# Performance work log

Measured on AMD Instinct MI355X. Metric: run time of the kernel, lower is better.

The kernel has to match this reference:

```python
import jax, jax.numpy as jnp
import numpy as np
import math

B, S, H, NH, NKV, HD = 1, 2048, 4096, 32, 8, 128
ROPE_THETA = 10000.0


def setup_inputs() -> dict:
    key = jax.random.key(0)
    ks = jax.random.split(key, 16)
    hidden_states = jax.random.normal(ks[0], (B, S, H), jnp.float32) * 0.02
    Wq = jax.random.normal(ks[1], (NH * HD, H), jnp.float32) * 0.02
    Wk = jax.random.normal(ks[2], (NKV * HD, H), jnp.float32) * 0.02
    Wv = jax.random.normal(ks[3], (NKV * HD, H), jnp.float32) * 0.02
    Wo = jax.random.normal(ks[4], (H, NH * HD), jnp.float32) * 0.02
    # RoPE cos/sin, HF Llama convention: emb = concat(freqs, freqs)
    inv_freq = 1.0 / (ROPE_THETA ** (jnp.arange(0, HD, 2, dtype=jnp.float32) / HD))
    pos = jnp.arange(S, dtype=jnp.float32)
    freqs = pos[:, None] * inv_freq[None, :]              # [S, HD/2]
    emb = jnp.concatenate([freqs, freqs], axis=-1)        # [S, HD]
    cos = jnp.cos(emb)[None]                              # [1, S, HD]
    sin = jnp.sin(emb)[None]
    # additive causal mask [B, 1, S, S]
    causal = jnp.tril(jnp.ones((S, S), dtype=bool))
    attention_mask = jnp.where(causal, 0.0, -1e9).astype(jnp.float32)[None, None]
    # reorder permutations (as written by GPTQ act-order reordering)
    perm = lambda k, n: jax.random.permutation(k, n).astype(jnp.int32)
    return {
        'hidden_states': hidden_states, 'Wq': Wq, 'Wk': Wk, 'Wv': Wv, 'Wo': Wo,
        'cos': cos, 'sin': sin, 'attention_mask': attention_mask,
        'q_order_col': perm(ks[5], H), 'q_order_row': perm(ks[6], NH * HD),
        'k_order_col': perm(ks[7], H), 'k_order_row': perm(ks[8], NKV * HD),
        'v_order_col': perm(ks[9], H), 'v_order_row': perm(ks[10], NKV * HD),
        'o_order_col': perm(ks[11], NH * HD), 'o_order_row': perm(ks[12], H),
    }


def _rotate_half(x):
    x1, x2 = jnp.split(x, 2, axis=-1)
    return jnp.concatenate([-x2, x1], axis=-1)


def reference(hidden_states, Wq, Wk, Wv, Wo, cos, sin, attention_mask,
              q_order_col, q_order_row, k_order_col, k_order_row,
              v_order_col, v_order_row, o_order_col, o_order_row):
    bsz, q_len, _ = hidden_states.shape
    # permuted projections: gather cols of input, GEMM, gather rows of output
    q = hidden_states[:, :, q_order_col] @ Wq.T
    q = q[:, :, q_order_row]
    k = hidden_states[:, :, k_order_col] @ Wk.T
    k = k[:, :, k_order_row]
    v = hidden_states[:, :, v_order_col] @ Wv.T
    v = v[:, :, v_order_row]
    q = q.reshape(bsz, q_len, NH, HD).transpose(0, 2, 1, 3)   # [B,NH,S,HD]
    k = k.reshape(bsz, q_len, NKV, HD).transpose(0, 2, 1, 3)  # [B,NKV,S,HD]
    v = v.reshape(bsz, q_len, NKV, HD).transpose(0, 2, 1, 3)
    # RoPE
    c = cos[:, None, :, :]  # [1,1,S,HD]
    s = sin[:, None, :, :]
    q = q * c + _rotate_half(q) * s
    k = k * c + _rotate_half(k) * s
    # repeat_kv for GQA
    rep = NH // NKV
    k = jnp.repeat(k, rep, axis=1)  # [B,NH,S,HD]
    v = jnp.repeat(v, rep, axis=1)
    # eager attention: full score matrix, fp32 softmax
    scores = jnp.einsum('bhqd,bhkd->bhqk', q, k) / math.sqrt(HD)
    scores = scores + attention_mask
    probs = jax.nn.softmax(scores.astype(jnp.float32), axis=-1).astype(q.dtype)
    # dropout p=0.0 (eval) -> identity
    attn = jnp.einsum('bhqk,bhkd->bhqd', probs, v)
    attn = attn.transpose(0, 2, 1, 3).reshape(bsz, q_len, NH * HD)
    out = attn[:, :, o_order_col] @ Wo.T
    out = out[:, :, o_order_row]
    return out
```

## Files before the change

### kernel.cpp

```cpp
#include <hip/hip_runtime.h>

typedef unsigned short u16;
typedef unsigned char u8;
typedef __bf16 bf16x8 __attribute__((ext_vector_type(8)));
typedef float f32x4 __attribute__((ext_vector_type(4)));
typedef int i32x4 __attribute__((ext_vector_type(4)));
typedef int i32x8 __attribute__((ext_vector_type(8)));

__device__ __forceinline__ u16 f2bf(float f) {
    unsigned u = __float_as_uint(f);
    unsigned r = (u + 0x7fffu + ((u >> 16) & 1u)) >> 16;
    return (u16)r;
}
__device__ __forceinline__ float bf2f(u16 h) {
    return __uint_as_float(((unsigned)h) << 16);
}
__device__ __forceinline__ unsigned pack_bf2(float lo, float hi) {
    unsigned a = __float_as_uint(hi) + 0x8000u;
    unsigned b = __float_as_uint(lo) + 0x8000u;
    return __builtin_amdgcn_perm(a, b, 0x07060302u);
}
__device__ __forceinline__ unsigned pack_fp8x4(float a, float b, float c, float d) {
    unsigned w = __builtin_amdgcn_cvt_pk_fp8_f32(a, b, 0, false);
    w = __builtin_amdgcn_cvt_pk_fp8_f32(c, d, w, true);
    return w;
}
__device__ __forceinline__ void async_copy16(const void* g, void* l) {
    __builtin_amdgcn_global_load_lds((__attribute__((address_space(1))) void*)(void*)g,
                                     (__attribute__((address_space(3))) void*)l, 16, 0, 0);
}

#define FP8_SCALE 64.0f
#define FP8_UNSCALE (1.0f / 4096.0f)


__global__ void inv4_k(const int* __restrict__ q, const int* __restrict__ k,
                       const int* __restrict__ v, const int* __restrict__ o,
                       int* __restrict__ invq, int* __restrict__ invk,
                       int* __restrict__ invv, int* __restrict__ invo) {
    int i = blockIdx.x * 256 + threadIdx.x;
    int a = i >> 12, j = i & 4095;
    const int* p = a == 0 ? q : a == 1 ? k : a == 2 ? v : o;
    int* inv = a == 0 ? invq : a == 1 ? invk : a == 2 ? invv : invo;
    inv[p[j]] = j;
}

__global__ __launch_bounds__(256) void permw4_k(
    const float* __restrict__ Wq, const float* __restrict__ Wk,
    const float* __restrict__ Wv, const float* __restrict__ Wo,
    const int* __restrict__ qor, const int* __restrict__ kor,
    const int* __restrict__ vor, const int* __restrict__ oor,
    const int* __restrict__ invq, const int* __restrict__ invk,
    const int* __restrict__ invv, const int* __restrict__ invo,
    u8* __restrict__ Wqkf8, u16* __restrict__ Wvp, u16* __restrict__ Wop) {
    __shared__ float rowbuf[4096];
    int j = blockIdx.x;
    const float* W; const int* rp; const int* inv; int row; int f8;
    u8* out8 = nullptr; u16* out16 = nullptr;
    if (j < 4096)      { W = Wq; rp = qor; inv = invq; row = j;        out8 = Wqkf8 + (size_t)j * 4096; f8 = 1; }
    else if (j < 5120) { W = Wk; rp = kor; inv = invk; row = j - 4096; out8 = Wqkf8 + (size_t)j * 4096; f8 = 1; }
    else if (j < 6144) { W = Wv; rp = vor; inv = invv; row = j - 5120; out16 = Wvp + (size_t)(j - 5120) * 4096; f8 = 0; }
    else               { W = Wo; rp = oor; inv = invo; row = j - 6144; out16 = Wop + (size_t)(j - 6144) * 4096; f8 = 0; }
    const float4* wr4 = (const float4*)(W + (size_t)rp[row] * 4096);
#pragma unroll
    for (int t = 0; t < 4; t++)
        ((float4*)rowbuf)[threadIdx.x + t * 256] = wr4[threadIdx.x + t * 256];
    __syncthreads();
    if (f8) {
        int t = threadIdx.x;
        const int4* inv4p = (const int4*)inv;
        float v[16];
#pragma unroll
        for (int u = 0; u < 4; u++) {
            int4 ix = inv4p[t * 4 + u];
            v[4 * u + 0] = rowbuf[ix.x] * FP8_SCALE;
            v[4 * u + 1] = rowbuf[ix.y] * FP8_SCALE;
            v[4 * u + 2] = rowbuf[ix.z] * FP8_SCALE;
            v[4 * u + 3] = rowbuf[ix.w] * FP8_SCALE;
        }
        uint4 wv;
        wv.x = pack_fp8x4(v[0], v[1], v[2], v[3]);
        wv.y = pack_fp8x4(v[4], v[5], v[6], v[7]);
        wv.z = pack_fp8x4(v[8], v[9], v[10], v[11]);
        wv.w = pack_fp8x4(v[12], v[13], v[14], v[15]);
        int tb = (t & ~7) | ((t & 7) ^ (j & 7));
        ((uint4*)out8)[tb] = wv;
    } else {
        unsigned* o32 = (unsigned*)out16;
        const int2* inv2 = (const int2*)inv;
#pragma unroll
        for (int t = 0; t < 8; t++) {
            int c = threadIdx.x + t * 256;
            int2 ij = inv2[c];
            o32[c] = pack_bf2(rowbuf[ij.x], rowbuf[ij.y]);
        }
    }
}

__global__ __launch_bounds__(256) void cvt_k(const float* __restrict__ x,
                                             u16* __restrict__ Xb,
                                             u8* __restrict__ Xf8) {
    int row = blockIdx.x;
    int t = threadIdx.x;
    const float4* src = (const float4*)(x + (size_t)row * 4096);
    float v[16];
#pragma unroll
    for (int u = 0; u < 4; u++) {
        float4 a = src[t * 4 + u];
        v[4 * u + 0] = a.x; v[4 * u + 1] = a.y; v[4 * u + 2] = a.z; v[4 * u + 3] = a.w;
    }
    uint4 b0, b1;
    b0.x = pack_bf2(v[0], v[1]);  b0.y = pack_bf2(v[2], v[3]);
    b0.z = pack_bf2(v[4], v[5]);  b0.w = pack_bf2(v[6], v[7]);
    b1.x = pack_bf2(v[8], v[9]);  b1.y = pack_bf2(v[10], v[11]);
    b1.z = pack_bf2(v[12], v[13]); b1.w = pack_bf2(v[14], v[15]);
    uint4* ob = (uint4*)(Xb + (size_t)row * 4096);
    ob[t * 2] = b0;
    ob[t * 2 + 1] = b1;
    uint4 w8;
    w8.x = pack_fp8x4(v[0] * FP8_SCALE, v[1] * FP8_SCALE, v[2] * FP8_SCALE, v[3] * FP8_SCALE);
    w8.y = pack_fp8x4(v[4] * FP8_SCALE, v[5] * FP8_SCALE, v[6] * FP8_SCALE, v[7] * FP8_SCALE);
    w8.z = pack_fp8x4(v[8] * FP8_SCALE, v[9] * FP8_SCALE, v[10] * FP8_SCALE, v[11] * FP8_SCALE);
    w8.w = pack_fp8x4(v[12] * FP8_SCALE, v[13] * FP8_SCALE, v[14] * FP8_SCALE, v[15] * FP8_SCALE);
    int tb = (t & ~7) | ((t & 7) ^ (row & 7));
    ((uint4*)(Xf8 + (size_t)row * 4096))[tb] = w8;
}

__global__ __launch_bounds__(256) void rope_tr_k(u16* __restrict__ X,
                                                 const float* __restrict__ cosv,
                                                 const float* __restrict__ sinv,
                                                 const float* __restrict__ Vpart,
                                                 u16* __restrict__ Vt) {
    __shared__ u16 t[64][65];
    if (blockIdx.x < 20480) {
        int tt = blockIdx.x * 256 + threadIdx.x;
        int d = tt & 63;
        int rest = tt >> 6;
        int head = rest % 40;
        int s = rest / 40;
        size_t base = (size_t)s * 6144 + head * 128 + d;
        float x1 = bf2f(X[base]), x2 = bf2f(X[base + 64]);
        float c1 = cosv[s * 128 + d], s1 = sinv[s * 128 + d];
        float c2 = cosv[s * 128 + d + 64], s2 = sinv[s * 128 + d + 64];
        float sc = head < 32 ? 0.08838834764831845f : 1.0f;
        X[base]      = f2bf((x1 * c1 - x2 * s1) * sc);
        X[base + 64] = f2bf((x2 * c2 + x1 * s2) * sc);
    } else {
        int bx = blockIdx.x - 20480;
        int s0 = (bx & 31) * 64, c0 = (bx >> 5) * 64;
        int x = threadIdx.x & 63, y4 = threadIdx.x >> 6;
        const float* Vp0 = Vpart;
        const float* Vp1 = Vpart + (size_t)2048 * 1024;
        for (int i = 0; i < 16; i++) {
            int r = y4 * 16 + i;
            size_t idx = (size_t)(s0 + r) * 1024 + c0 + x;
            t[r][x] = f2bf(Vp0[idx] + Vp1[idx]);
        }
        __syncthreads();
        for (int i = 0; i < 16; i++) {
            int r = y4 * 16 + i;
            int xk = 4 * (x & 15) + (x >> 4);
            Vt[(size_t)(c0 + r) * 2048 + s0 + xk] = t[x][r];
        }
    }
}


__global__ __launch_bounds__(256) void gemm_qkv_k(const u8* __restrict__ Xf8,
                                                  const u16* __restrict__ Xb,
                                                  const u8* __restrict__ Wqk,
                                                  const u16* __restrict__ Wv,
                                                  u16* __restrict__ QKV,
                                                  float* __restrict__ Vpart) {
    __shared__ u8 lds[32768];
    const int tid = threadIdx.x;
    const int w = tid >> 6, lane = tid & 63;
    const int quad = lane >> 4, l16 = lane & 15;
    const int bm0 = blockIdx.y * 128;
    const int wm = (w >> 1) * 64, wn = (w & 1) * 64;
    if (blockIdx.x < 40) {
        const int bn0 = blockIdx.x * 128;
        u8* ldsA = lds;
        u8* ldsB = lds + 16384;
        const u8* Ag = Xf8 + (size_t)(bm0 + w * 32 + (lane >> 3)) * 4096 + (lane & 7) * 16;
        const u8* Bg = Wqk + (size_t)(bn0 + w * 32 + (lane >> 3)) * 4096 + (lane & 7) * 16;
        u8* la = ldsA + w * 32 * 128;
        u8* lb = ldsB + w * 32 * 128;
        const int swz = l16 & 7;
        f32x4 acc[4][4] = {};
        for (int k0 = 0; k0 < 4096; k0 += 128) {
#pragma unroll
            for (int t = 0; t < 4; t++) async_copy16(Ag + (size_t)t * 8 * 4096 + k0, la + t * 1024);
#pragma unroll
            for (int t = 0; t < 4; t++) async_copy16(Bg + (size_t)t * 8 * 4096 + k0, lb + t * 1024);
            __syncthreads();
            i32x8 af[4], bf[4];
#pragma unroll
            for (int i = 0; i < 4; i++) {
                int r = wm + i * 16 + l16;
                union { i32x8 v8; i32x4 v4[2]; } u;
                u.v4[0] = *(const i32x4*)&ldsA[r * 128 + ((quad * 2) ^ swz) * 16];
                u.v4[1] = *(const i32x4*)&ldsA[r * 128 + ((quad * 2 + 1) ^ swz) * 16];
                af[i] = u.v8;
            }
#pragma unroll
            for (int j = 0; j < 4; j++) {
                int r = wn + j * 16 + l16;
                union { i32x8 v8; i32x4 v4[2]; } u;
                u.v4[0] = *(const i32x4*)&ldsB[r * 128 + ((quad * 2) ^ swz) * 16];
                u.v4[1] = *(const i32x4*)&ldsB[r * 128 + ((quad * 2 + 1) ^ swz) * 16];
                bf[j] = u.v8;
            }
#pragma unroll
            for (int i = 0; i < 4; i++)
#pragma unroll
                for (int j = 0; j < 4; j++)
                    acc[i][j] = __builtin_amdgcn_mfma_scale_f32_16x16x128_f8f6f4(
                        af[i], bf[j], acc[i][j], 0, 0,
                        0, 0x7F7F7F7F, 0, 0x7F7F7F7F);
            __syncthreads();
        }
#pragma unroll
        for (int i = 0; i < 4; i++) {
            const int row = bm0 + wm + i * 16 + quad * 4;
#pragma unroll
            for (int j = 0; j < 4; j++) {
                const int col = bn0 + wn + j * 16 + l16;
#pragma unroll
                for (int r = 0; r < 4; r++)
                    QKV[(size_t)(row + r) * 6144 + col] = f2bf(acc[i][j][r] * FP8_UNSCALE);
            }
        }
    } else {
        const int vx = blockIdx.x - 40;
        const int bn0 = (vx & 7) * 128;
        const int kslice = vx >> 3;
        const int kb = kslice * 2048;
        u16* lds_a0 = (u16*)lds;
        u16* lds_a1 = (u16*)(lds + 8192);
        u16* lds_b0 = (u16*)(lds + 16384);
        u16* lds_b1 = (u16*)(lds + 24576);
        const int r0 = w * 16 + (lane >> 2);
        const int c0 = (lane & 3) * 8;
        const u16* Ag = Xb + (size_t)(bm0 + r0) * 4096 + kb + c0;
        const u16* Bg = Wv + (size_t)(bn0 + r0) * 4096 + kb + c0;
        f32x4 acc[4][4] = {};
        for (int k0 = 0; k0 < 2048; k0 += 64) {
            async_copy16(Ag + k0,                         lds_a0 + w * 512);
            async_copy16(Ag + (size_t)64 * 4096 + k0,     lds_a0 + (w + 4) * 512);
            async_copy16(Ag + k0 + 32,                    lds_a1 + w * 512);
            async_copy16(Ag + (size_t)64 * 4096 + k0 + 32, lds_a1 + (w + 4) * 512);
            async_copy16(Bg + k0,                         lds_b0 + w * 512);
            async_copy16(Bg + (size_t)64 * 4096 + k0,     lds_b0 + (w + 4) * 512);
            async_copy16(Bg + k0 + 32,                    lds_b1 + w * 512);
            async_copy16(Bg + (size_t)64 * 4096 + k0 + 32, lds_b1 + (w + 4) * 512);
            __syncthreads();
#pragma unroll
            for (int kk = 0; kk < 2; kk++) {
                const u16* la = kk ? lds_a1 : lds_a0;
                const u16* lb = kk ? lds_b1 : lds_b0;
                bf16x8 af[4], bfv[4];
#pragma unroll
                for (int i = 0; i < 4; i++)
                    af[i] = *(const bf16x8*)&la[(wm + i * 16 + l16) * 32 + quad * 8];
#pragma unroll
                for (int j = 0; j < 4; j++)
                    bfv[j] = *(const bf16x8*)&lb[(wn + j * 16 + l16) * 32 + quad * 8];
#pragma unroll
                for (int i = 0; i < 4; i++)
#pragma unroll
                    for (int j = 0; j < 4; j++)
                        acc[i][j] = __builtin_amdgcn_mfma_f32_16x16x32_bf16(af[i], bfv[j], acc[i][j], 0, 0, 0);
            }
            __syncthreads();
        }
        float* Vp = Vpart + (size_t)kslice * 2048 * 1024;
#pragma unroll
        for (int i = 0; i < 4; i++) {
            const int row = bm0 + wm + i * 16 + quad * 4;
#pragma unroll
            for (int j = 0; j < 4; j++) {
                const int col = bn0 + wn + j * 16 + l16;
#pragma unroll
                for (int r = 0; r < 4; r++)
                    Vp[(size_t)(row + r) * 1024 + col] = acc[i][j][r];
            }
        }
    }
}


__global__ __launch_bounds__(256) void gemm_o_k(const u16* __restrict__ A,
                                                const u16* __restrict__ B,
                                                float* __restrict__ Opart) {
    __shared__ u16 lds[16384];
    u16* lds_a0 = lds;
    u16* lds_a1 = lds + 4096;
    u16* lds_b0 = lds + 8192;
    u16* lds_b1 = lds + 12288;
    const int tid = threadIdx.x;
    const int w = tid >> 6, lane = tid & 63;
    const int quad = lane >> 4, l16 = lane & 15;
    const int bm0 = blockIdx.y * 128;
    const int bn0 = (blockIdx.x & 31) * 128;
    const int kslice = blockIdx.x >> 5;
    const int kb = kslice * 2048;
    const int wm = (w >> 1) * 64, wn = (w & 1) * 64;
    const int r0 = w * 16 + (lane >> 2);
    const int c0 = (lane & 3) * 8;
    const u16* Ag = A + (size_t)(bm0 + r0) * 4096 + kb + c0;
    const u16* Bg = B + (size_t)(bn0 + r0) * 4096 + kb + c0;
    f32x4 acc[4][4] = {};
    for (int k0 = 0; k0 < 2048; k0 += 64) {
        async_copy16(Ag + k0,                          lds_a0 + w * 512);
        async_copy16(Ag + (size_t)64 * 4096 + k0,      lds_a0 + (w + 4) * 512);
        async_copy16(Ag + k0 + 32,                     lds_a1 + w * 512);
        async_copy16(Ag + (size_t)64 * 4096 + k0 + 32, lds_a1 + (w + 4) * 512);
        async_copy16(Bg + k0,                          lds_b0 + w * 512);
        async_copy16(Bg + (size_t)64 * 4096 + k0,      lds_b0 + (w + 4) * 512);
        async_copy16(Bg + k0 + 32,                     lds_b1 + w * 512);
        async_copy16(Bg + (size_t)64 * 4096 + k0 + 32, lds_b1 + (w + 4) * 512);
        __syncthreads();
#pragma unroll
        for (int kk = 0; kk < 2; kk++) {
            const u16* la = kk ? lds_a1 : lds_a0;
            const u16* lb = kk ? lds_b1 : lds_b0;
            bf16x8 af[4], bfv[4];
#pragma unroll
            for (int i = 0; i < 4; i++)
                af[i] = *(const bf16x8*)&la[(wm + i * 16 + l16) * 32 + quad * 8];
#pragma unroll
            for (int j = 0; j < 4; j++)
                bfv[j] = *(const bf16x8*)&lb[(wn + j * 16 + l16) * 32 + quad * 8];
#pragma unroll
            for (int i = 0; i < 4; i++)
#pragma unroll
                for (int j = 0; j < 4; j++)
                    acc[i][j] = __builtin_amdgcn_mfma_f32_16x16x32_bf16(af[i], bfv[j], acc[i][j], 0, 0, 0);
        }
        __syncthreads();
    }
    float* Op = Opart + (size_t)kslice * 2048 * 4096;
#pragma unroll
    for (int i = 0; i < 4; i++) {
        const int row = bm0 + wm + i * 16 + quad * 4;
#pragma unroll
        for (int j = 0; j < 4; j++) {
            const int col = bn0 + wn + j * 16 + l16;
#pragma unroll
            for (int r = 0; r < 4; r++)
                Op[(size_t)(row + r) * 4096 + col] = acc[i][j][r];
        }
    }
}

__global__ void reduce_k(const float* __restrict__ P, float* __restrict__ out) {
    size_t i = (size_t)blockIdx.x * 256 + threadIdx.x;
    float4 a = ((const float4*)P)[i];
    float4 b = ((const float4*)(P + (size_t)2048 * 4096))[i];
    float4 r;
    r.x = a.x + b.x; r.y = a.y + b.y; r.z = a.z + b.z; r.w = a.w + b.w;
    ((float4*)out)[i] = r;
}


__global__ __launch_bounds__(256) void attn_k(const u16* __restrict__ Qb,
                                              const u16* __restrict__ Kb,
                                              const u16* __restrict__ Vt,
                                              u16* __restrict__ Ob,
                                              int qstride, int kstride) {
    __shared__ u16 ldsK[4 * 64 * 32];
    __shared__ u16 ldsV[2 * 128 * 32];
    __shared__ u16 ldsP[4][32 * 72];
    const int h = blockIdx.x;
    const int qt = (int)gridDim.y - 1 - (int)blockIdx.y;
    const int kvh = h >> 2;
    const int tid = threadIdx.x;
    const int w = tid >> 6, lane = tid & 63;
    const int quad = lane >> 4, l16 = lane & 15;
    const int q0 = qt * 128;
    const int wrow = q0 + w * 32;

    bf16x8 qf[2][4];
#pragma unroll
    for (int mi = 0; mi < 2; mi++)
#pragma unroll
        for (int kk = 0; kk < 4; kk++)
            qf[mi][kk] = *(const bf16x8*)&Qb[(size_t)(wrow + mi * 16 + l16) * qstride +
                                             h * 128 + kk * 32 + quad * 8];

    const u16* kp[4]; const u16* vp[4];
    u16* ldk[4]; u16* ldv[4];
#pragma unroll
    for (int t = 0; t < 4; t++) {
        int wl = w + t * 4;
        int kk = wl >> 2, part = wl & 3;
        kp[t] = Kb + (size_t)(part * 16 + (lane >> 2)) * kstride + kvh * 128 + kk * 32 + (lane & 3) * 8;
        int ks2 = wl >> 3, p2 = wl & 7;
        vp[t] = Vt + (size_t)(kvh * 128 + p2 * 16 + (lane >> 2)) * 2048 + ks2 * 32 + (lane & 3) * 8;
        ldk[t] = ldsK + wl * 512;
        ldv[t] = ldsV + wl * 512;
    }

    f32x4 acc_o[2][8] = {};
    float lrow[2][4] = {};

    const int nk = 2 * (qt + 1);
    for (int kn = 0; kn < nk; kn++) {
        const int g0 = kn * 64;
#pragma unroll
        for (int t = 0; t < 4; t++) async_copy16(kp[t], ldk[t]);
#pragma unroll
        for (int t = 0; t < 4; t++) async_copy16(vp[t], ldv[t]);
#pragma unroll
        for (int t = 0; t < 4; t++) { kp[t] += (size_t)64 * kstride; vp[t] += 64; }
        __syncthreads();

        if (g0 <= wrow + 31) {
            f32x4 accs[2][4] = {};
#pragma unroll
            for (int kk = 0; kk < 4; kk++) {
                bf16x8 bfrag[4];
#pragma unroll
                for (int ni = 0; ni < 4; ni++)
                    bfrag[ni] = *(const bf16x8*)&ldsK[kk * 2048 + (ni * 16 + l16) * 32 + quad * 8];
#pragma unroll
                for (int mi = 0; mi < 2; mi++)
#pragma unroll
                    for (int ni = 0; ni < 4; ni++)
                        accs[mi][ni] = __builtin_amdgcn_mfma_f32_16x16x32_bf16(
                            qf[mi][kk], bfrag[ni], accs[mi][ni], 0, 0, 0);
            }
            const bool diag = (g0 + 63 > wrow);
            int kidx[4];
#pragma unroll
            for (int ni = 0; ni < 4; ni++) kidx[ni] = g0 + ni * 16 + l16;
#pragma unroll
            for (int mi = 0; mi < 2; mi++) {
#pragma unroll
                for (int r = 0; r < 4; r++) {
                    const int qrow = wrow + mi * 16 + quad * 4 + r;
                    float p[4];
#pragma unroll
                    for (int ni = 0; ni < 4; ni++) {
                        float s = accs[mi][ni][r];
                        if (diag && (kidx[ni] > qrow)) s = -1e30f;
                        p[ni] = __expf(s);
                    }
                    lrow[mi][r] += (p[0] + p[1]) + (p[2] + p[3]);
                    uint2 pk;
                    pk.x = pack_bf2(p[0], p[1]);
                    pk.y = pack_bf2(p[2], p[3]);
                    *(uint2*)&ldsP[w][(mi * 16 + quad * 4 + r) * 72 + l16 * 4] = pk;
                }
            }
#pragma unroll
            for (int ks = 0; ks < 2; ks++) {
                bf16x8 pa[2];
#pragma unroll
                for (int mi = 0; mi < 2; mi++)
                    pa[mi] = *(const bf16x8*)&ldsP[w][(mi * 16 + l16) * 72 + ks * 32 + quad * 8];
#pragma unroll
                for (int oj = 0; oj < 8; oj++) {
                    bf16x8 vb = *(const bf16x8*)&ldsV[ks * 4096 + (oj * 16 + l16) * 32 + quad * 8];
#pragma unroll
                    for (int mi = 0; mi < 2; mi++)
                        acc_o[mi][oj] = __builtin_amdgcn_mfma_f32_16x16x32_bf16(
                            pa[mi], vb, acc_o[mi][oj], 0, 0, 0);
                }
            }
        }
        __syncthreads();
    }
#pragma unroll
    for (int mi = 0; mi < 2; mi++)
#pragma unroll
        for (int r = 0; r < 4; r++) {
            float l = lrow[mi][r];
            l += __shfl_xor(l, 1);
            l += __shfl_xor(l, 2);
            l += __shfl_xor(l, 4);
            l += __shfl_xor(l, 8);
            const float inv = 1.0f / l;
            const int qrow = wrow + mi * 16 + quad * 4 + r;
#pragma unroll
            for (int oj = 0; oj < 8; oj++)
                Ob[(size_t)qrow * 4096 + h * 128 + oj * 16 + l16] =
                    f2bf(acc_o[mi][oj][r] * inv);
        }
}


extern "C" void kernel_launch(void* const* d_in, const int* in_sizes, int n_in,
                              void* d_out, int out_size, void* d_ws, size_t ws_size,
                              hipStream_t stream) {
    (void)in_sizes; (void)n_in; (void)out_size; (void)ws_size;
    const float* hidden = (const float*)d_in[0];
    const float* Wq = (const float*)d_in[1];
    const float* Wk = (const float*)d_in[2];
    const float* Wv = (const float*)d_in[3];
    const float* Wo = (const float*)d_in[4];
    const float* cosv = (const float*)d_in[5];
    const float* sinv = (const float*)d_in[6];
    const int* qoc = (const int*)d_in[8];
    const int* qor = (const int*)d_in[9];
    const int* koc = (const int*)d_in[10];
    const int* kor = (const int*)d_in[11];
    const int* voc = (const int*)d_in[12];
    const int* vor = (const int*)d_in[13];
    const int* ooc = (const int*)d_in[14];
    const int* oor = (const int*)d_in[15];

    char* ws = (char*)d_ws;
    size_t off = 0;
    int* invq = (int*)(ws + off); off += 16384;
    int* invk = (int*)(ws + off); off += 16384;
    int* invv = (int*)(ws + off); off += 16384;
    int* invo = (int*)(ws + off); off += 16384;
    u16* Wop   = (u16*)(ws + off); off += (size_t)4096 * 4096 * 2;
    u16* Xb    = (u16*)(ws + off); off += (size_t)2048 * 4096 * 2;
    size_t trans = off;
    u8*  Wqkf8 = (u8*)(ws + off);  off += (size_t)5120 * 4096;
    u16* Wvp   = (u16*)(ws + off); off += (size_t)1024 * 4096 * 2;
    u8*  Xf8   = (u8*)(ws + off);  off += (size_t)2048 * 4096;
    u16* QKVb  = (u16*)(ws + off); off += (size_t)2048 * 6144 * 2;
    u16* Vtb   = (u16*)(ws + off); off += (size_t)1024 * 2048 * 2;
    float* Vpart = (float*)(ws + off); off += (size_t)2 * 2048 * 1024 * 4;
    float* Opart = (float*)(ws + trans);
    u16* Attb  = Xb;

    inv4_k<<<64, 256, 0, stream>>>(qoc, koc, voc, ooc, invq, invk, invv, invo);
    permw4_k<<<10240, 256, 0, stream>>>(Wq, Wk, Wv, Wo, qor, kor, vor, oor,
                                        invq, invk, invv, invo, Wqkf8, Wvp, Wop);
    cvt_k<<<2048, 256, 0, stream>>>(hidden, Xb, Xf8);

    gemm_qkv_k<<<dim3(56, 16), 256, 0, stream>>>(Xf8, Xb, Wqkf8, Wvp, QKVb, Vpart);

    rope_tr_k<<<20992, 256, 0, stream>>>(QKVb, cosv, sinv, Vpart, Vtb);

    attn_k<<<dim3(32, 16), 256, 0, stream>>>(QKVb, QKVb + 4096, Vtb, Attb, 6144, 6144);

    gemm_o_k<<<dim3(64, 16), 256, 0, stream>>>(Attb, Wop, Opart);
    reduce_k<<<8192, 256, 0, stream>>>(Opart, (float*)d_out);
}
```

Measured before the change: 526.6 us.

## Fuse RoPE into QKV GEMM epilogue and atomic-add O split-K into output

Q/K weight rows are reordered during weight permutation so that each RoPE pair (d, d+64) lands in accumulator tiles held by the same lane. That lets the QKV GEMM epilogue apply RoPE and the Q scale directly, and the separate rope pass over QKV is removed. The output projection's two K-slices now atomically add into a zeroed output instead of writing partials and running a reduce kernel. This saves the extra global read/write passes, at the cost of atomics, a memset, and nondeterministic summation order.

```diff
diff --git a/kernel.cpp b/kernel.cpp
--- a/kernel.cpp
+++ b/kernel.cpp
@@ -61,6 +61,10 @@
     else if (j < 5120) { W = Wk; rp = kor; inv = invk; row = j - 4096; out8 = Wqkf8 + (size_t)j * 4096; f8 = 1; }
     else if (j < 6144) { W = Wv; rp = vor; inv = invv; row = j - 5120; out16 = Wvp + (size_t)(j - 5120) * 4096; f8 = 0; }
     else               { W = Wo; rp = oor; inv = invo; row = j - 6144; out16 = Wop + (size_t)(j - 6144) * 4096; f8 = 0; }
+    if (f8) {
+        int hd = row & 127, b = hd >> 4;
+        row = (row & ~127) | ((hd & 15) | ((b & 1) << 6) | ((b & 2) << 3) | ((hd & 64) >> 1));
+    }
     const float4* wr4 = (const float4*)(W + (size_t)rp[row] * 4096);
 #pragma unroll
     for (int t = 0; t < 4; t++)
@@ -126,42 +130,24 @@
     ((uint4*)(Xf8 + (size_t)row * 4096))[tb] = w8;
 }
 
-__global__ __launch_bounds__(256) void rope_tr_k(u16* __restrict__ X,
-                                                 const float* __restrict__ cosv,
-                                                 const float* __restrict__ sinv,
-                                                 const float* __restrict__ Vpart,
-                                                 u16* __restrict__ Vt) {
+__global__ __launch_bounds__(256) void vtr_k(const float* __restrict__ Vpart,
+                                             u16* __restrict__ Vt) {
     __shared__ u16 t[64][65];
-    if (blockIdx.x < 20480) {
-        int tt = blockIdx.x * 256 + threadIdx.x;
-        int d = tt & 63;
-        int rest = tt >> 6;
-        int head = rest % 40;
-        int s = rest / 40;
-        size_t base = (size_t)s * 6144 + head * 128 + d;
-        float x1 = bf2f(X[base]), x2 = bf2f(X[base + 64]);
-        float c1 = cosv[s * 128 + d], s1 = sinv[s * 128 + d];
-        float c2 = cosv[s * 128 + d + 64], s2 = sinv[s * 128 + d + 64];
-        float sc = head < 32 ? 0.08838834764831845f : 1.0f;
-        X[base]      = f2bf((x1 * c1 - x2 * s1) * sc);
-        X[base + 64] = f2bf((x2 * c2 + x1 * s2) * sc);
-    } else {
-        int bx = blockIdx.x - 20480;
-        int s0 = (bx & 31) * 64, c0 = (bx >> 5) * 64;
-        int x = threadIdx.x & 63, y4 = threadIdx.x >> 6;
-        const float* Vp0 = Vpart;
-        const float* Vp1 = Vpart + (size_t)2048 * 1024;
-        for (int i = 0; i < 16; i++) {
-            int r = y4 * 16 + i;
-            size_t idx = (size_t)(s0 + r) * 1024 + c0 + x;
-            t[r][x] = f2bf(Vp0[idx] + Vp1[idx]);
-        }
-        __syncthreads();
-        for (int i = 0; i < 16; i++) {
-            int r = y4 * 16 + i;
-            int xk = 4 * (x & 15) + (x >> 4);
-            Vt[(size_t)(c0 + r) * 2048 + s0 + xk] = t[x][r];
-        }
+    int bx = blockIdx.x;
+    int s0 = (bx & 31) * 64, c0 = (bx >> 5) * 64;
+    int x = threadIdx.x & 63, y4 = threadIdx.x >> 6;
+    const float* Vp0 = Vpart;
+    const float* Vp1 = Vpart + (size_t)2048 * 1024;
+    for (int i = 0; i < 16; i++) {
+        int r = y4 * 16 + i;
+        size_t idx = (size_t)(s0 + r) * 1024 + c0 + x;
+        t[r][x] = f2bf(Vp0[idx] + Vp1[idx]);
+    }
+    __syncthreads();
+    for (int i = 0; i < 16; i++) {
+        int r = y4 * 16 + i;
+        int xk = 4 * (x & 15) + (x >> 4);
+        Vt[(size_t)(c0 + r) * 2048 + s0 + xk] = t[x][r];
     }
 }
 
@@ -171,7 +157,9 @@
                                                   const u8* __restrict__ Wqk,
                                                   const u16* __restrict__ Wv,
                                                   u16* __restrict__ QKV,
-                                                  float* __restrict__ Vpart) {
+                                                  float* __restrict__ Vpart,
+                                                  const float* __restrict__ cosv,
+                                                  const float* __restrict__ sinv) {
     __shared__ u8 lds[32768];
     const int tid = threadIdx.x;
     const int w = tid >> 6, lane = tid & 63;
@@ -220,15 +208,25 @@
                         0, 0x7F7F7F7F, 0, 0x7F7F7F7F);
             __syncthreads();
         }
+        const float qsc = (bn0 < 4096) ? 0.08838834764831845f : 1.0f;
+        const int hb = (wn ? 32 : 0) + l16;
 #pragma unroll
         for (int i = 0; i < 4; i++) {
             const int row = bm0 + wm + i * 16 + quad * 4;
 #pragma unroll
-            for (int j = 0; j < 4; j++) {
-                const int col = bn0 + wn + j * 16 + l16;
-#pragma unroll
-                for (int r = 0; r < 4; r++)
-                    QKV[(size_t)(row + r) * 6144 + col] = f2bf(acc[i][j][r] * FP8_UNSCALE);
+            for (int jp = 0; jp < 2; jp++) {
+                const int d1 = hb + jp * 16;
+                const int ce = bn0 + wn + jp * 32 + l16;
+#pragma unroll
+                for (int r = 0; r < 4; r++) {
+                    const int s = row + r;
+                    const float c  = cosv[s * 128 + d1];
+                    const float sn = sinv[s * 128 + d1];
+                    const float x1 = acc[i][jp * 2][r]     * FP8_UNSCALE;
+                    const float x2 = acc[i][jp * 2 + 1][r] * FP8_UNSCALE;
+                    QKV[(size_t)s * 6144 + ce]      = f2bf((x1 * c - x2 * sn) * qsc);
+                    QKV[(size_t)s * 6144 + ce + 16] = f2bf((x2 * c + x1 * sn) * qsc);
+                }
             }
         }
     } else {
@@ -292,7 +290,7 @@
 
 __global__ __launch_bounds__(256) void gemm_o_k(const u16* __restrict__ A,
                                                 const u16* __restrict__ B,
-                                                float* __restrict__ Opart) {
+                                                float* __restrict__ Out) {
     __shared__ u16 lds[16384];
     u16* lds_a0 = lds;
     u16* lds_a1 = lds + 4096;
@@ -340,7 +338,6 @@
         }
         __syncthreads();
     }
-    float* Op = Opart + (size_t)kslice * 2048 * 4096;
 #pragma unroll
     for (int i = 0; i < 4; i++) {
         const int row = bm0 + wm + i * 16 + quad * 4;
@@ -349,18 +346,9 @@
             const int col = bn0 + wn + j * 16 + l16;
 #pragma unroll
             for (int r = 0; r < 4; r++)
-                Op[(size_t)(row + r) * 4096 + col] = acc[i][j][r];
-        }
-    }
-}
-
-__global__ void reduce_k(const float* __restrict__ P, float* __restrict__ out) {
-    size_t i = (size_t)blockIdx.x * 256 + threadIdx.x;
-    float4 a = ((const float4*)P)[i];
-    float4 b = ((const float4*)(P + (size_t)2048 * 4096))[i];
-    float4 r;
-    r.x = a.x + b.x; r.y = a.y + b.y; r.z = a.z + b.z; r.w = a.w + b.w;
-    ((float4*)out)[i] = r;
+                unsafeAtomicAdd(&Out[(size_t)(row + r) * 4096 + col], acc[i][j][r]);
+        }
+    }
 }
 
 
@@ -519,14 +507,12 @@
     int* invo = (int*)(ws + off); off += 16384;
     u16* Wop   = (u16*)(ws + off); off += (size_t)4096 * 4096 * 2;
     u16* Xb    = (u16*)(ws + off); off += (size_t)2048 * 4096 * 2;
-    size_t trans = off;
     u8*  Wqkf8 = (u8*)(ws + off);  off += (size_t)5120 * 4096;
     u16* Wvp   = (u16*)(ws + off); off += (size_t)1024 * 4096 * 2;
     u8*  Xf8   = (u8*)(ws + off);  off += (size_t)2048 * 4096;
     u16* QKVb  = (u16*)(ws + off); off += (size_t)2048 * 6144 * 2;
     u16* Vtb   = (u16*)(ws + off); off += (size_t)1024 * 2048 * 2;
     float* Vpart = (float*)(ws + off); off += (size_t)2 * 2048 * 1024 * 4;
-    float* Opart = (float*)(ws + trans);
     u16* Attb  = Xb;
 
     inv4_k<<<64, 256, 0, stream>>>(qoc, koc, voc, ooc, invq, invk, invv, invo);
@@ -534,12 +520,13 @@
                                         invq, invk, invv, invo, Wqkf8, Wvp, Wop);
     cvt_k<<<2048, 256, 0, stream>>>(hidden, Xb, Xf8);
 
-    gemm_qkv_k<<<dim3(56, 16), 256, 0, stream>>>(Xf8, Xb, Wqkf8, Wvp, QKVb, Vpart);
-
-    rope_tr_k<<<20992, 256, 0, stream>>>(QKVb, cosv, sinv, Vpart, Vtb);
+    gemm_qkv_k<<<dim3(56, 16), 256, 0, stream>>>(Xf8, Xb, Wqkf8, Wvp, QKVb, Vpart,
+                                                 cosv, sinv);
+
+    vtr_k<<<512, 256, 0, stream>>>(Vpart, Vtb);
 
     attn_k<<<dim3(32, 16), 256, 0, stream>>>(QKVb, QKVb + 4096, Vtb, Attb, 6144, 6144);
 
-    gemm_o_k<<<dim3(64, 16), 256, 0, stream>>>(Attb, Wop, Opart);
-    reduce_k<<<8192, 256, 0, stream>>>(Opart, (float*)d_out);
-}
+    hipMemsetAsync(d_out, 0, (size_t)2048 * 4096 * sizeof(float), stream);
+    gemm_o_k<<<dim3(64, 16), 256, 0, stream>>>(Attb, Wop, (float*)d_out);
+}
```

Result: no change. 528.6 us (+0.4%).
